# Kernel optimization log

Hardware: AMD Instinct MI355X
Metric: run time of the kernel (lower is better)

## Reference

```python
import jax, jax.numpy as jnp
import numpy as np

EPS = 1e-4  # ProtoPNet epsilon in distance-to-similarity transform


def setup_inputs() -> dict:
    key = jax.random.key(0)
    k1, k2, k3 = jax.random.split(key, 3)
    B, C, T = 128, 128, 777   # backbone feature map [B, C, T]
    P, NC = 500, 5            # prototypes, classes
    x = jax.random.normal(k1, (B, C, T), dtype=jnp.float32)
    prototypes = jax.random.uniform(k2, (P, C), dtype=jnp.float32)
    last_w = jax.random.normal(k3, (P, NC), dtype=jnp.float32)
    return {"x": x, "prototypes": prototypes, "last_w": last_w}


def reference(x, prototypes, last_w):
    # Prototype layer via the conv-trick L2 expansion:
    x2 = jnp.sum(x * x, axis=1)                      # [B, T]
    p2 = jnp.sum(prototypes * prototypes, axis=1)    # [P]
    xp = jnp.einsum('bct,pc->bpt', x, prototypes)    # [B, P, T]  (dominant GEMM)
    d = jnp.maximum(x2[:, None, :] - 2.0 * xp + p2[None, :, None], 0.0)  # [B, P, T]
    # Min-pool over all patches (global min over temporal axis)
    min_d = jnp.min(d, axis=2)                       # [B, P]
    # Distance -> similarity: log((d + 1) / (d + eps))
    sim = jnp.log((min_d + 1.0) / (min_d + EPS))     # [B, P]
    # Final evidence layer
    logits = sim @ last_w                            # [B, num_classes]
    return logits
```

## Files before the change

kernel.cpp:

```cpp
#include <hip/hip_runtime.h>
#include <hip/hip_bf16.h>

#define B_DIM 128
#define C_DIM 128
#define T_DIM 777
#define P_DIM 500
#define P_PAD 512
#define NCLS  5
#define EPSV  1e-4f
#define NT    25

typedef unsigned short u16;
typedef unsigned int   u32;
typedef __attribute__((ext_vector_type(8))) short short8;
typedef __attribute__((ext_vector_type(4))) float f32x4;
typedef float float4u __attribute__((ext_vector_type(4), aligned(4)));

__device__ __forceinline__ u32 cvt_pk_bf16(float a, float b) {
    u32 r;
    asm("v_cvt_pk_bf16_f32 %0, %1, %2" : "=v"(r) : "v"(a), "v"(b));
    return r;
}

__global__ __launch_bounds__(256, 3) void fused_gemm_min(
    const float* __restrict__ x,
    const float* __restrict__ proto,
    float* __restrict__ wsmin) {

    const int o   = blockIdx.x;
    const int xcd = o & 7, j = o >> 3;
    const int bl  = j / 6;
    const int r6  = j - bl * 6;
    const int b   = xcd * 16 + bl;
    const int pt  = r6 & 1;
    const int th  = r6 >> 1;
    const int it0 = (th == 0) ? 0 : (th == 1 ? 9 : 17);
    const int itN = (th == 0) ? 9 : (th == 1 ? 17 : NT);

    const int tid = threadIdx.x;
    const int w = tid >> 6, l = tid & 63;
    const int row16 = l & 15, kq = l >> 4;
    const int wp = pt * 256 + w * 64;

    const int c0  = (tid >> 3) << 2;
    const int tl0 = (tid & 7) << 2;

    __shared__ __align__(16) char  smem[2][32 * 256];
    __shared__ __align__(16) float x2p[2][4][32];

    const float* xb = x + (size_t)b * C_DIM * T_DIM;

    short8 afr[4][4];
#pragma unroll
    for (int ps = 0; ps < 4; ++ps) {
        const int r = wp + ps * 16 + row16;
#pragma unroll
        for (int kst = 0; kst < 4; ++kst) {
            const int k0 = kst * 32 + kq * 8;
            union { short8 s; u32 d[4]; } t;
            if (r < P_DIM) {
                float4 u0 = *(const float4*)(proto + r * C_DIM + k0);
                float4 u1 = *(const float4*)(proto + r * C_DIM + k0 + 4);
                t.d[0] = cvt_pk_bf16(u0.x, u0.y);
                t.d[1] = cvt_pk_bf16(u0.z, u0.w);
                t.d[2] = cvt_pk_bf16(u1.x, u1.y);
                t.d[3] = cvt_pk_bf16(u1.z, u1.w);
            } else {
                t.d[0] = t.d[1] = t.d[2] = t.d[3] = 0u;
            }
            afr[ps][kst] = t.s;
        }
    }

    float vb[4][4];
    auto loadv = [&](int it) {
        const int tb = it * 32 + tl0;
        if (tb + 3 < T_DIM) {
#pragma unroll
            for (int r = 0; r < 4; ++r) {
                float4u u = *(const float4u*)(xb + (c0 + r) * T_DIM + tb);
                vb[r][0]=u[0]; vb[r][1]=u[1]; vb[r][2]=u[2]; vb[r][3]=u[3];
            }
        } else {
#pragma unroll
            for (int r = 0; r < 4; ++r)
#pragma unroll
                for (int jj = 0; jj < 4; ++jj) {
                    const int t = tb + jj;
                    vb[r][jj] = (t < T_DIM) ? xb[(c0 + r) * T_DIM + t] : 0.f;
                }
        }
    };

    auto write_tile = [&](int it, int bsel) {
        const int t0 = it * 32;
        float s[4];
#pragma unroll
        for (int jj = 0; jj < 4; ++jj)
            s[jj] = vb[0][jj]*vb[0][jj] + vb[1][jj]*vb[1][jj]
                  + vb[2][jj]*vb[2][jj] + vb[3][jj]*vb[3][jj];
#pragma unroll
        for (int jj = 0; jj < 4; ++jj) {
            const u32 lo = cvt_pk_bf16(vb[0][jj], vb[1][jj]);
            const u32 hi = cvt_pk_bf16(vb[2][jj], vb[3][jj]);
            const int tl  = tl0 + jj;
            const int off = tl * 256 + (((c0 >> 3) ^ (tl & 7)) << 4) + ((c0 & 4) << 1);
            *(uint2*)(smem[bsel] + off) = make_uint2(lo, hi);
        }
#pragma unroll
        for (int m = 8; m <= 32; m <<= 1)
#pragma unroll
            for (int jj = 0; jj < 4; ++jj) s[jj] += __shfl_xor(s[jj], m);
        if ((l >> 3) == 0) {
            float4 o4;
            o4.x = (t0 + tl0 + 0 < T_DIM) ? s[0] : 1e30f;
            o4.y = (t0 + tl0 + 1 < T_DIM) ? s[1] : 1e30f;
            o4.z = (t0 + tl0 + 2 < T_DIM) ? s[2] : 1e30f;
            o4.w = (t0 + tl0 + 3 < T_DIM) ? s[3] : 1e30f;
            *(float4*)(&x2p[bsel][w][tl0]) = o4;
        }
    };

    f32x4 minv[4];
#pragma unroll
    for (int ps = 0; ps < 4; ++ps) minv[ps] = (f32x4){1e30f, 1e30f, 1e30f, 1e30f};

    loadv(it0);
    write_tile(it0, 0);
    __syncthreads();

    int cur = 0;
    for (int it = it0; it < itN; ++it) {
        const bool more = (it + 1 < itN);
        if (more) loadv(it + 1);

        f32x4 acc[4][2];
#pragma unroll
        for (int ps = 0; ps < 4; ++ps)
#pragma unroll
            for (int ts = 0; ts < 2; ++ts) acc[ps][ts] = (f32x4){0.f, 0.f, 0.f, 0.f};

        const char* sbase = smem[cur];
        __builtin_amdgcn_s_setprio(1);
#pragma unroll
        for (int kst = 0; kst < 4; ++kst) {
            short8 bfr[2];
#pragma unroll
            for (int ts = 0; ts < 2; ++ts) {
                const int tl = ts * 16 + row16;
                const int gr = (kst * 4 + kq) ^ (tl & 7);
                bfr[ts] = *(const short8*)(sbase + tl * 256 + (gr << 4));
            }
#pragma unroll
            for (int ps = 0; ps < 4; ++ps)
#pragma unroll
                for (int ts = 0; ts < 2; ++ts)
                    acc[ps][ts] = __builtin_amdgcn_mfma_f32_16x16x32_bf16(
                        afr[ps][kst], bfr[ts], acc[ps][ts], 0, 0, 0);
        }
        __builtin_amdgcn_s_setprio(0);

        const float x2v0 = x2p[cur][0][row16]      + x2p[cur][1][row16]
                         + x2p[cur][2][row16]      + x2p[cur][3][row16];
        const float x2v1 = x2p[cur][0][16 + row16] + x2p[cur][1][16 + row16]
                         + x2p[cur][2][16 + row16] + x2p[cur][3][16 + row16];
#pragma unroll
        for (int ps = 0; ps < 4; ++ps)
#pragma unroll
            for (int q = 0; q < 4; ++q) {
                minv[ps][q] = fminf(minv[ps][q], fmaf(-2.f, acc[ps][0][q], x2v0));
                minv[ps][q] = fminf(minv[ps][q], fmaf(-2.f, acc[ps][1][q], x2v1));
            }

        if (more) write_tile(it + 1, cur ^ 1);
        __syncthreads();
        cur ^= 1;
    }

#pragma unroll
    for (int m = 1; m <= 8; m <<= 1)
#pragma unroll
        for (int ps = 0; ps < 4; ++ps)
#pragma unroll
            for (int q = 0; q < 4; ++q)
                minv[ps][q] = fminf(minv[ps][q], __shfl_xor(minv[ps][q], m));

    if (row16 == 0) {
#pragma unroll
        for (int ps = 0; ps < 4; ++ps) {
            const int p = wp + ps * 16 + kq * 4;
            *(float4*)(&wsmin[((size_t)th * B_DIM + b) * P_PAD + p]) =
                make_float4(minv[ps][0], minv[ps][1], minv[ps][2], minv[ps][3]);
        }
    }
}

__global__ __launch_bounds__(256) void combine_logits(
    const float* __restrict__ proto, const float* __restrict__ lw,
    const float* __restrict__ wsmin, float* __restrict__ out) {
    const int b = blockIdx.x, tid = threadIdx.x;
    float a[NCLS] = {0.f, 0.f, 0.f, 0.f, 0.f};
    for (int p = tid; p < P_DIM; p += 256) {
        const float4* pr = (const float4*)(proto + p * C_DIM);
        float p2 = 0.f;
#pragma unroll
        for (int i = 0; i < 32; ++i) {
            float4 u = pr[i];
            p2 += u.x*u.x + u.y*u.y + u.z*u.z + u.w*u.w;
        }
        const float m0 = wsmin[(0 * B_DIM + b) * P_PAD + p];
        const float m1 = wsmin[(1 * B_DIM + b) * P_PAD + p];
        const float m2 = wsmin[(2 * B_DIM + b) * P_PAD + p];
        const float m  = fminf(fminf(m0, m1), m2);
        const float md = fmaxf(m + p2, 0.f);
        const float sim = logf((md + 1.f) / (md + EPSV));
#pragma unroll
        for (int n = 0; n < NCLS; ++n) a[n] = fmaf(sim, lw[p * NCLS + n], a[n]);
    }
#pragma unroll
    for (int m = 1; m <= 32; m <<= 1)
#pragma unroll
        for (int n = 0; n < NCLS; ++n) a[n] += __shfl_xor(a[n], m);
    __shared__ float red[4][NCLS];
    const int w = tid >> 6, l = tid & 63;
    if (l == 0) {
#pragma unroll
        for (int n = 0; n < NCLS; ++n) red[w][n] = a[n];
    }
    __syncthreads();
    if (tid < NCLS)
        out[b * NCLS + tid] = red[0][tid] + red[1][tid] + red[2][tid] + red[3][tid];
}

__global__ __launch_bounds__(256) void fallback_k(const float* __restrict__ x,
                                                  const float* __restrict__ proto,
                                                  const float* __restrict__ lw,
                                                  float* __restrict__ out) {
    __shared__ float x2s[T_DIM];
    __shared__ float sims[P_DIM];
    int b = blockIdx.x, tid = threadIdx.x;
    for (int t = tid; t < T_DIM; t += 256) {
        float a = 0.f;
        for (int c = 0; c < C_DIM; ++c) { float v = x[((size_t)b * C_DIM + c) * T_DIM + t]; a = fmaf(v, v, a); }
        x2s[t] = a;
    }
    __syncthreads();
    for (int p = tid; p < P_DIM; p += 256) {
        float p2 = 0.f;
        for (int c = 0; c < C_DIM; ++c) { float v = proto[p * C_DIM + c]; p2 = fmaf(v, v, p2); }
        float mind = 1e30f;
        for (int t = 0; t < T_DIM; ++t) {
            float xp = 0.f;
            for (int c = 0; c < C_DIM; ++c)
                xp = fmaf(x[((size_t)b * C_DIM + c) * T_DIM + t], proto[p * C_DIM + c], xp);
            float d = fmaxf(x2s[t] - 2.f * xp + p2, 0.f);
            mind = fminf(mind, d);
        }
        sims[p] = logf((mind + 1.f) / (mind + EPSV));
    }
    __syncthreads();
    if (tid < NCLS) {
        float a = 0.f;
        for (int p = 0; p < P_DIM; ++p) a = fmaf(sims[p], lw[p * NCLS + tid], a);
        out[b * NCLS + tid] = a;
    }
}

extern "C" void kernel_launch(void* const* d_in, const int* in_sizes, int n_in,
                              void* d_out, int out_size, void* d_ws, size_t ws_size,
                              hipStream_t stream) {
    const float* x     = (const float*)d_in[0];
    const float* proto = (const float*)d_in[1];
    const float* lw    = (const float*)d_in[2];
    float* out = (float*)d_out;

    const size_t need = (size_t)3 * B_DIM * P_PAD * sizeof(float);

    if (ws_size >= need) {
        float* wsmin = (float*)d_ws;
        fused_gemm_min<<<dim3(768), 256, 0, stream>>>(x, proto, wsmin);
        combine_logits<<<dim3(B_DIM), 256, 0, stream>>>(proto, lw, wsmin, out);
    } else {
        fallback_k<<<dim3(B_DIM), 256, 0, stream>>>(x, proto, lw, out);
    }
}
```

Baseline: 50.77 us.

## Split x preprocessing into separate bf16 transpose kernel feeding GEMM-min

Adds a prep kernel that converts x to bf16, transposes it to [B, T_pad, C] and computes per-position squared norms into workspace. The GEMM-min kernel then streams pre-swizzled int4 tiles straight into a single LDS buffer instead of converting fp32 strided data inline. This targets the per-block conversion and norm-reduction work and the uncoalesced fp32 loads inside the main loop. In exchange it adds a kernel launch and an extra round trip of about 27 MB through global memory, and drops the double-buffered LDS in favour of two barriers per iteration.

Measured after the change: 54.71 us. +7.7%, slower.

```diff
diff --git a/kernel.cpp b/kernel.cpp
--- a/kernel.cpp
+++ b/kernel.cpp
@@ -4,17 +4,23 @@
 #define B_DIM 128
 #define C_DIM 128
 #define T_DIM 777
+#define T_PAD 832
 #define P_DIM 500
 #define P_PAD 512
 #define NCLS  5
 #define EPSV  1e-4f
-#define NT    25
+#define NTILE 26
 
 typedef unsigned short u16;
 typedef unsigned int   u32;
 typedef __attribute__((ext_vector_type(8))) short short8;
 typedef __attribute__((ext_vector_type(4))) float f32x4;
-typedef float float4u __attribute__((ext_vector_type(4), aligned(4)));
+
+__device__ __forceinline__ u16 f2bf(float f) {
+    u32 u = __float_as_uint(f);
+    u += 0x7FFFu + ((u >> 16) & 1u);
+    return (u16)(u >> 16);
+}
 
 __device__ __forceinline__ u32 cvt_pk_bf16(float a, float b) {
     u32 r;
@@ -22,8 +28,41 @@
     return r;
 }
 
-__global__ __launch_bounds__(256, 3) void fused_gemm_min(
-    const float* __restrict__ x,
+__global__ __launch_bounds__(256) void prep_x(const float* __restrict__ x,
+                                              u16* __restrict__ xbf,
+                                              float* __restrict__ x2) {
+    const int tc = blockIdx.x;
+    const int b  = blockIdx.y;
+    const int tid = threadIdx.x, w = tid >> 6, l = tid & 63;
+    __shared__ __align__(16) u16 xt[64][136];
+    const int t_loc = w * 16 + (l & 15);
+    const int cg = l >> 4;
+    const int t = tc * 64 + t_loc;
+    const float* xb = x + (size_t)b * C_DIM * T_DIM;
+    float acc = 0.f;
+#pragma unroll 8
+    for (int c0 = 0; c0 < C_DIM; c0 += 4) {
+        int c = c0 + cg;
+        float v = (t < T_DIM) ? xb[c * T_DIM + t] : 0.f;
+        acc = fmaf(v, v, acc);
+        xt[t_loc][c] = f2bf(v);
+    }
+    acc += __shfl_xor(acc, 16);
+    acc += __shfl_xor(acc, 32);
+    if (cg == 0) x2[b * T_PAD + t] = (t < T_DIM) ? acc : 1e30f;
+    __syncthreads();
+    int4* dst = (int4*)(xbf + ((size_t)b * T_PAD + tc * 64) * C_DIM);
+#pragma unroll
+    for (int q = 0; q < 4; ++q) {
+        int f = q * 256 + tid;
+        int tr = f >> 4, g = f & 15;
+        dst[f] = *(const int4*)((const char*)xt + tr * 272 + g * 16);
+    }
+}
+
+__global__ __launch_bounds__(256, 3) void gemm_min(
+    const int4* __restrict__ xg,
+    const float* __restrict__ x2,
     const float* __restrict__ proto,
     float* __restrict__ wsmin) {
 
@@ -35,20 +74,14 @@
     const int pt  = r6 & 1;
     const int th  = r6 >> 1;
     const int it0 = (th == 0) ? 0 : (th == 1 ? 9 : 17);
-    const int itN = (th == 0) ? 9 : (th == 1 ? 17 : NT);
+    const int itN = (th == 0) ? 9 : (th == 1 ? 17 : NTILE);
 
     const int tid = threadIdx.x;
     const int w = tid >> 6, l = tid & 63;
     const int row16 = l & 15, kq = l >> 4;
     const int wp = pt * 256 + w * 64;
 
-    const int c0  = (tid >> 3) << 2;
-    const int tl0 = (tid & 7) << 2;
-
-    __shared__ __align__(16) char  smem[2][32 * 256];
-    __shared__ __align__(16) float x2p[2][4][32];
-
-    const float* xb = x + (size_t)b * C_DIM * T_DIM;
+    __shared__ __align__(16) char smem[32 * 256];
 
     short8 afr[4][4];
 #pragma unroll
@@ -72,67 +105,33 @@
         }
     }
 
-    float vb[4][4];
-    auto loadv = [&](int it) {
-        const int tb = it * 32 + tl0;
-        if (tb + 3 < T_DIM) {
-#pragma unroll
-            for (int r = 0; r < 4; ++r) {
-                float4u u = *(const float4u*)(xb + (c0 + r) * T_DIM + tb);
-                vb[r][0]=u[0]; vb[r][1]=u[1]; vb[r][2]=u[2]; vb[r][3]=u[3];
-            }
-        } else {
-#pragma unroll
-            for (int r = 0; r < 4; ++r)
-#pragma unroll
-                for (int jj = 0; jj < 4; ++jj) {
-                    const int t = tb + jj;
-                    vb[r][jj] = (t < T_DIM) ? xb[(c0 + r) * T_DIM + t] : 0.f;
-                }
-        }
-    };
-
-    auto write_tile = [&](int it, int bsel) {
-        const int t0 = it * 32;
-        float s[4];
-#pragma unroll
-        for (int jj = 0; jj < 4; ++jj)
-            s[jj] = vb[0][jj]*vb[0][jj] + vb[1][jj]*vb[1][jj]
-                  + vb[2][jj]*vb[2][jj] + vb[3][jj]*vb[3][jj];
-#pragma unroll
-        for (int jj = 0; jj < 4; ++jj) {
-            const u32 lo = cvt_pk_bf16(vb[0][jj], vb[1][jj]);
-            const u32 hi = cvt_pk_bf16(vb[2][jj], vb[3][jj]);
-            const int tl  = tl0 + jj;
-            const int off = tl * 256 + (((c0 >> 3) ^ (tl & 7)) << 4) + ((c0 & 4) << 1);
-            *(uint2*)(smem[bsel] + off) = make_uint2(lo, hi);
-        }
-#pragma unroll
-        for (int m = 8; m <= 32; m <<= 1)
-#pragma unroll
-            for (int jj = 0; jj < 4; ++jj) s[jj] += __shfl_xor(s[jj], m);
-        if ((l >> 3) == 0) {
-            float4 o4;
-            o4.x = (t0 + tl0 + 0 < T_DIM) ? s[0] : 1e30f;
-            o4.y = (t0 + tl0 + 1 < T_DIM) ? s[1] : 1e30f;
-            o4.z = (t0 + tl0 + 2 < T_DIM) ? s[2] : 1e30f;
-            o4.w = (t0 + tl0 + 3 < T_DIM) ? s[3] : 1e30f;
-            *(float4*)(&x2p[bsel][w][tl0]) = o4;
-        }
-    };
+    const int d0 = (tid >> 4) * 256 + ((((tid & 15) ^ ((tid >> 4) & 7))) << 4);
+    const int d1 = d0 + 4096;
+    const int4* gb = xg + (size_t)b * T_PAD * 16;
+    const float* x2b = x2 + b * T_PAD;
 
     f32x4 minv[4];
 #pragma unroll
     for (int ps = 0; ps < 4; ++ps) minv[ps] = (f32x4){1e30f, 1e30f, 1e30f, 1e30f};
 
-    loadv(it0);
-    write_tile(it0, 0);
-    __syncthreads();
-
-    int cur = 0;
+    int4 v0 = gb[it0 * 512 + tid];
+    int4 v1 = gb[it0 * 512 + 256 + tid];
+    float xa = x2b[it0 * 32 + row16];
+    float xc = x2b[it0 * 32 + 16 + row16];
+
     for (int it = it0; it < itN; ++it) {
-        const bool more = (it + 1 < itN);
-        if (more) loadv(it + 1);
+        __syncthreads();
+        *(int4*)(smem + d0) = v0;
+        *(int4*)(smem + d1) = v1;
+        __syncthreads();
+
+        const float cxa = xa, cxc = xc;
+        if (it + 1 < itN) {
+            v0 = gb[(it + 1) * 512 + tid];
+            v1 = gb[(it + 1) * 512 + 256 + tid];
+            xa = x2b[(it + 1) * 32 + row16];
+            xc = x2b[(it + 1) * 32 + 16 + row16];
+        }
 
         f32x4 acc[4][2];
 #pragma unroll
@@ -140,7 +139,6 @@
 #pragma unroll
             for (int ts = 0; ts < 2; ++ts) acc[ps][ts] = (f32x4){0.f, 0.f, 0.f, 0.f};
 
-        const char* sbase = smem[cur];
         __builtin_amdgcn_s_setprio(1);
 #pragma unroll
         for (int kst = 0; kst < 4; ++kst) {
@@ -149,7 +147,7 @@
             for (int ts = 0; ts < 2; ++ts) {
                 const int tl = ts * 16 + row16;
                 const int gr = (kst * 4 + kq) ^ (tl & 7);
-                bfr[ts] = *(const short8*)(sbase + tl * 256 + (gr << 4));
+                bfr[ts] = *(const short8*)(smem + tl * 256 + (gr << 4));
             }
 #pragma unroll
             for (int ps = 0; ps < 4; ++ps)
@@ -160,21 +158,13 @@
         }
         __builtin_amdgcn_s_setprio(0);
 
-        const float x2v0 = x2p[cur][0][row16]      + x2p[cur][1][row16]
-                         + x2p[cur][2][row16]      + x2p[cur][3][row16];
-        const float x2v1 = x2p[cur][0][16 + row16] + x2p[cur][1][16 + row16]
-                         + x2p[cur][2][16 + row16] + x2p[cur][3][16 + row16];
 #pragma unroll
         for (int ps = 0; ps < 4; ++ps)
 #pragma unroll
             for (int q = 0; q < 4; ++q) {
-                minv[ps][q] = fminf(minv[ps][q], fmaf(-2.f, acc[ps][0][q], x2v0));
-                minv[ps][q] = fminf(minv[ps][q], fmaf(-2.f, acc[ps][1][q], x2v1));
+                minv[ps][q] = fminf(minv[ps][q], fmaf(-2.f, acc[ps][0][q], cxa));
+                minv[ps][q] = fminf(minv[ps][q], fmaf(-2.f, acc[ps][1][q], cxc));
             }
-
-        if (more) write_tile(it + 1, cur ^ 1);
-        __syncthreads();
-        cur ^= 1;
     }
 
 #pragma unroll
@@ -274,12 +264,18 @@
     const float* lw    = (const float*)d_in[2];
     float* out = (float*)d_out;
 
-    const size_t need = (size_t)3 * B_DIM * P_PAD * sizeof(float);
+    const size_t xbf_bytes = (size_t)B_DIM * T_PAD * C_DIM * 2;
+    const size_t x2_off  = xbf_bytes;
+    const size_t min_off = x2_off + (size_t)B_DIM * T_PAD * 4;
+    const size_t need    = min_off + (size_t)3 * B_DIM * P_PAD * 4;
 
     if (ws_size >= need) {
-        float* wsmin = (float*)d_ws;
-        fused_gemm_min<<<dim3(768), 256, 0, stream>>>(x, proto, wsmin);
-        combine_logits<<<dim3(B_DIM), 256, 0, stream>>>(proto, lw, wsmin, out);
+        u16*   xbf   = (u16*)d_ws;
+        float* x2    = (float*)((char*)d_ws + x2_off);
+        float* wsmin = (float*)((char*)d_ws + min_off);
+        prep_x        <<<dim3(T_PAD / 64, B_DIM), 256, 0, stream>>>(x, xbf, x2);
+        gemm_min      <<<dim3(768),               256, 0, stream>>>((const int4*)xbf, x2, proto, wsmin);
+        combine_logits<<<dim3(B_DIM),             256, 0, stream>>>(proto, lw, wsmin, out);
     } else {
         fallback_k<<<dim3(B_DIM), 256, 0, stream>>>(x, proto, lw, out);
     }
```

## Use 64-wide T tiles, 2-way T split, and precompute x norms up front

Applied to the files above, without the earlier changes.

Widens each loop iteration's time tile from 32 to 64 columns, so each wave issues 16 MFMAs per k-step. It cuts the temporal split from three blocks to two, shrinking the grid from 768 to 512 blocks and the combine reads from three partial minima to two. Squared x norms are now computed in a prologue by a strided scalar loop over channels, not fused into the tile write. The double-buffered LDS is replaced with a single buffer guarded by two barriers per iteration. This lowers the per-tile overhead ratio but adds a serial, uncoalesced-ish prologue that rereads x, and it removes the overlap between the LDS write and compute.

Result: faster. 48.76 us (-4.0%).

```diff
diff --git a/kernel.cpp b/kernel.cpp
--- a/kernel.cpp
+++ b/kernel.cpp
@@ -8,7 +8,8 @@
 #define P_PAD 512
 #define NCLS  5
 #define EPSV  1e-4f
-#define NT    25
+#define NTILE 13
+#define SPLIT 7
 
 typedef unsigned short u16;
 typedef unsigned int   u32;
@@ -22,20 +23,19 @@
     return r;
 }
 
-__global__ __launch_bounds__(256, 3) void fused_gemm_min(
+__global__ __launch_bounds__(256, 2) void fused_gemm_min(
     const float* __restrict__ x,
     const float* __restrict__ proto,
     float* __restrict__ wsmin) {
 
     const int o   = blockIdx.x;
     const int xcd = o & 7, j = o >> 3;
-    const int bl  = j / 6;
-    const int r6  = j - bl * 6;
-    const int b   = xcd * 16 + bl;
-    const int pt  = r6 & 1;
-    const int th  = r6 >> 1;
-    const int it0 = (th == 0) ? 0 : (th == 1 ? 9 : 17);
-    const int itN = (th == 0) ? 9 : (th == 1 ? 17 : NT);
+    const int b   = xcd * 16 + (j >> 2);
+    const int pt  = (j >> 1) & 1, th = j & 1;
+    const int it0 = th ? SPLIT : 0;
+    const int itN = th ? NTILE : SPLIT;
+    const int tb0 = it0 * 64;
+    const int nT  = (itN - it0) * 64;
 
     const int tid = threadIdx.x;
     const int w = tid >> 6, l = tid & 63;
@@ -45,10 +45,25 @@
     const int c0  = (tid >> 3) << 2;
     const int tl0 = (tid & 7) << 2;
 
-    __shared__ __align__(16) char  smem[2][32 * 256];
-    __shared__ __align__(16) float x2p[2][4][32];
+    __shared__ __align__(16) char  smem[64 * 256];
+    __shared__ __align__(16) float x2s[448];
 
     const float* xb = x + (size_t)b * C_DIM * T_DIM;
+
+    for (int i = tid; i < nT; i += 256) {
+        const int t = tb0 + i;
+        float a = 0.f;
+        if (t < T_DIM) {
+#pragma unroll 8
+            for (int c = 0; c < C_DIM; ++c) {
+                const float v = xb[c * T_DIM + t];
+                a = fmaf(v, v, a);
+            }
+            x2s[i] = a;
+        } else {
+            x2s[i] = 1e30f;
+        }
+    }
 
     short8 afr[4][4];
 #pragma unroll
@@ -72,109 +87,90 @@
         }
     }
 
-    float vb[4][4];
+    float vb[2][4][4];
     auto loadv = [&](int it) {
-        const int tb = it * 32 + tl0;
-        if (tb + 3 < T_DIM) {
-#pragma unroll
-            for (int r = 0; r < 4; ++r) {
-                float4u u = *(const float4u*)(xb + (c0 + r) * T_DIM + tb);
-                vb[r][0]=u[0]; vb[r][1]=u[1]; vb[r][2]=u[2]; vb[r][3]=u[3];
-            }
-        } else {
-#pragma unroll
-            for (int r = 0; r < 4; ++r)
-#pragma unroll
-                for (int jj = 0; jj < 4; ++jj) {
-                    const int t = tb + jj;
-                    vb[r][jj] = (t < T_DIM) ? xb[(c0 + r) * T_DIM + t] : 0.f;
+#pragma unroll
+        for (int h = 0; h < 2; ++h) {
+            const int tb = it * 64 + h * 32 + tl0;
+            if (tb + 3 < T_DIM) {
+#pragma unroll
+                for (int r = 0; r < 4; ++r) {
+                    float4u u = *(const float4u*)(xb + (c0 + r) * T_DIM + tb);
+                    vb[h][r][0]=u[0]; vb[h][r][1]=u[1]; vb[h][r][2]=u[2]; vb[h][r][3]=u[3];
                 }
+            } else {
+#pragma unroll
+                for (int r = 0; r < 4; ++r)
+#pragma unroll
+                    for (int jj = 0; jj < 4; ++jj) {
+                        const int t = (tb + jj < T_DIM) ? (tb + jj) : (T_DIM - 1);
+                        vb[h][r][jj] = xb[(c0 + r) * T_DIM + t];
+                    }
+            }
         }
     };
 
-    auto write_tile = [&](int it, int bsel) {
-        const int t0 = it * 32;
-        float s[4];
-#pragma unroll
-        for (int jj = 0; jj < 4; ++jj)
-            s[jj] = vb[0][jj]*vb[0][jj] + vb[1][jj]*vb[1][jj]
-                  + vb[2][jj]*vb[2][jj] + vb[3][jj]*vb[3][jj];
-#pragma unroll
-        for (int jj = 0; jj < 4; ++jj) {
-            const u32 lo = cvt_pk_bf16(vb[0][jj], vb[1][jj]);
-            const u32 hi = cvt_pk_bf16(vb[2][jj], vb[3][jj]);
-            const int tl  = tl0 + jj;
-            const int off = tl * 256 + (((c0 >> 3) ^ (tl & 7)) << 4) + ((c0 & 4) << 1);
-            *(uint2*)(smem[bsel] + off) = make_uint2(lo, hi);
-        }
-#pragma unroll
-        for (int m = 8; m <= 32; m <<= 1)
-#pragma unroll
-            for (int jj = 0; jj < 4; ++jj) s[jj] += __shfl_xor(s[jj], m);
-        if ((l >> 3) == 0) {
-            float4 o4;
-            o4.x = (t0 + tl0 + 0 < T_DIM) ? s[0] : 1e30f;
-            o4.y = (t0 + tl0 + 1 < T_DIM) ? s[1] : 1e30f;
-            o4.z = (t0 + tl0 + 2 < T_DIM) ? s[2] : 1e30f;
-            o4.w = (t0 + tl0 + 3 < T_DIM) ? s[3] : 1e30f;
-            *(float4*)(&x2p[bsel][w][tl0]) = o4;
-        }
-    };
-
     f32x4 minv[4];
 #pragma unroll
     for (int ps = 0; ps < 4; ++ps) minv[ps] = (f32x4){1e30f, 1e30f, 1e30f, 1e30f};
 
+    __syncthreads();
     loadv(it0);
-    write_tile(it0, 0);
-    __syncthreads();
-
-    int cur = 0;
+
     for (int it = it0; it < itN; ++it) {
-        const bool more = (it + 1 < itN);
-        if (more) loadv(it + 1);
-
-        f32x4 acc[4][2];
+#pragma unroll
+        for (int h = 0; h < 2; ++h)
+#pragma unroll
+            for (int jj = 0; jj < 4; ++jj) {
+                const u32 lo = cvt_pk_bf16(vb[h][0][jj], vb[h][1][jj]);
+                const u32 hi = cvt_pk_bf16(vb[h][2][jj], vb[h][3][jj]);
+                const int tl  = h * 32 + tl0 + jj;
+                const int off = tl * 256 + (((c0 >> 3) ^ (tl & 7)) << 4) + ((c0 & 4) << 1);
+                *(uint2*)(smem + off) = make_uint2(lo, hi);
+            }
+        __syncthreads();
+
+        if (it + 1 < itN) loadv(it + 1);
+
+        float xv[4];
+#pragma unroll
+        for (int ts = 0; ts < 4; ++ts)
+            xv[ts] = x2s[(it - it0) * 64 + ts * 16 + row16];
+
+        f32x4 acc[4][4];
 #pragma unroll
         for (int ps = 0; ps < 4; ++ps)
 #pragma unroll
-            for (int ts = 0; ts < 2; ++ts) acc[ps][ts] = (f32x4){0.f, 0.f, 0.f, 0.f};
-
-        const char* sbase = smem[cur];
+            for (int ts = 0; ts < 4; ++ts) acc[ps][ts] = (f32x4){0.f, 0.f, 0.f, 0.f};
+
         __builtin_amdgcn_s_setprio(1);
 #pragma unroll
         for (int kst = 0; kst < 4; ++kst) {
-            short8 bfr[2];
-#pragma unroll
-            for (int ts = 0; ts < 2; ++ts) {
+            short8 bfr[4];
+#pragma unroll
+            for (int ts = 0; ts < 4; ++ts) {
                 const int tl = ts * 16 + row16;
                 const int gr = (kst * 4 + kq) ^ (tl & 7);
-                bfr[ts] = *(const short8*)(sbase + tl * 256 + (gr << 4));
+                bfr[ts] = *(const short8*)(smem + tl * 256 + (gr << 4));
             }
 #pragma unroll
             for (int ps = 0; ps < 4; ++ps)
 #pragma unroll
-                for (int ts = 0; ts < 2; ++ts)
+                for (int ts = 0; ts < 4; ++ts)
                     acc[ps][ts] = __builtin_amdgcn_mfma_f32_16x16x32_bf16(
                         afr[ps][kst], bfr[ts], acc[ps][ts], 0, 0, 0);
         }
         __builtin_amdgcn_s_setprio(0);
 
-        const float x2v0 = x2p[cur][0][row16]      + x2p[cur][1][row16]
-                         + x2p[cur][2][row16]      + x2p[cur][3][row16];
-        const float x2v1 = x2p[cur][0][16 + row16] + x2p[cur][1][16 + row16]
-                         + x2p[cur][2][16 + row16] + x2p[cur][3][16 + row16];
 #pragma unroll
         for (int ps = 0; ps < 4; ++ps)
 #pragma unroll
-            for (int q = 0; q < 4; ++q) {
-                minv[ps][q] = fminf(minv[ps][q], fmaf(-2.f, acc[ps][0][q], x2v0));
-                minv[ps][q] = fminf(minv[ps][q], fmaf(-2.f, acc[ps][1][q], x2v1));
-            }
-
-        if (more) write_tile(it + 1, cur ^ 1);
+            for (int ts = 0; ts < 4; ++ts)
+#pragma unroll
+                for (int q = 0; q < 4; ++q)
+                    minv[ps][q] = fminf(minv[ps][q], fmaf(-2.f, acc[ps][ts][q], xv[ts]));
+
         __syncthreads();
-        cur ^= 1;
     }
 
 #pragma unroll
@@ -210,8 +206,7 @@
         }
         const float m0 = wsmin[(0 * B_DIM + b) * P_PAD + p];
         const float m1 = wsmin[(1 * B_DIM + b) * P_PAD + p];
-        const float m2 = wsmin[(2 * B_DIM + b) * P_PAD + p];
-        const float m  = fminf(fminf(m0, m1), m2);
+        const float m  = fminf(m0, m1);
         const float md = fmaxf(m + p2, 0.f);
         const float sim = logf((md + 1.f) / (md + EPSV));
 #pragma unroll
@@ -274,11 +269,11 @@
     const float* lw    = (const float*)d_in[2];
     float* out = (float*)d_out;
 
-    const size_t need = (size_t)3 * B_DIM * P_PAD * sizeof(float);
+    const size_t need = (size_t)2 * B_DIM * P_PAD * sizeof(float);
 
     if (ws_size >= need) {
         float* wsmin = (float*)d_ws;
-        fused_gemm_min<<<dim3(768), 256, 0, stream>>>(x, proto, wsmin);
+        fused_gemm_min<<<dim3(512), 256, 0, stream>>>(x, proto, wsmin);
         combine_logits<<<dim3(B_DIM), 256, 0, stream>>>(proto, lw, wsmin, out);
     } else {
         fallback_k<<<dim3(B_DIM), 256, 0, stream>>>(x, proto, lw, out);
```

## Split time axis four ways and single-buffer LDS for higher occupancy

Applied to the files above, without the earlier changes.

The temporal axis is now split into four chunks instead of three, giving 1024 blocks, and launch bounds are raised to four blocks per SM. The LDS double buffer becomes a single buffer with an extra barrier per iteration. The combine kernel reduces four partial minima instead of three. The goal is more parallelism and occupancy, at the cost of losing load/compute overlap through the second buffer, an extra sync per tile, and more blocks that each redo the prototype fragment load.

After: 97.92 us. 92.9% more time.

```diff
diff --git a/kernel.cpp b/kernel.cpp
--- a/kernel.cpp
+++ b/kernel.cpp
@@ -22,20 +22,19 @@
     return r;
 }
 
-__global__ __launch_bounds__(256, 3) void fused_gemm_min(
+__global__ __launch_bounds__(256, 4) void fused_gemm_min(
     const float* __restrict__ x,
     const float* __restrict__ proto,
     float* __restrict__ wsmin) {
 
     const int o   = blockIdx.x;
     const int xcd = o & 7, j = o >> 3;
-    const int bl  = j / 6;
-    const int r6  = j - bl * 6;
-    const int b   = xcd * 16 + bl;
-    const int pt  = r6 & 1;
-    const int th  = r6 >> 1;
-    const int it0 = (th == 0) ? 0 : (th == 1 ? 9 : 17);
-    const int itN = (th == 0) ? 9 : (th == 1 ? 17 : NT);
+    const int b   = xcd * 16 + (j >> 3);
+    const int r   = j & 7;
+    const int pt  = r >> 2;
+    const int th  = r & 3;
+    const int it0 = (th == 0) ? 0 : (th == 1 ? 7 : (th == 2 ? 13 : 19));
+    const int itN = (th == 0) ? 7 : (th == 1 ? 13 : (th == 2 ? 19 : NT));
 
     const int tid = threadIdx.x;
     const int w = tid >> 6, l = tid & 63;
@@ -45,22 +44,22 @@
     const int c0  = (tid >> 3) << 2;
     const int tl0 = (tid & 7) << 2;
 
-    __shared__ __align__(16) char  smem[2][32 * 256];
-    __shared__ __align__(16) float x2p[2][4][32];
+    __shared__ __align__(16) char  smem[32 * 256];
+    __shared__ __align__(16) float x2p[4][32];
 
     const float* xb = x + (size_t)b * C_DIM * T_DIM;
 
     short8 afr[4][4];
 #pragma unroll
     for (int ps = 0; ps < 4; ++ps) {
-        const int r = wp + ps * 16 + row16;
+        const int rr = wp + ps * 16 + row16;
 #pragma unroll
         for (int kst = 0; kst < 4; ++kst) {
             const int k0 = kst * 32 + kq * 8;
             union { short8 s; u32 d[4]; } t;
-            if (r < P_DIM) {
-                float4 u0 = *(const float4*)(proto + r * C_DIM + k0);
-                float4 u1 = *(const float4*)(proto + r * C_DIM + k0 + 4);
+            if (rr < P_DIM) {
+                float4 u0 = *(const float4*)(proto + rr * C_DIM + k0);
+                float4 u1 = *(const float4*)(proto + rr * C_DIM + k0 + 4);
                 t.d[0] = cvt_pk_bf16(u0.x, u0.y);
                 t.d[1] = cvt_pk_bf16(u0.z, u0.w);
                 t.d[2] = cvt_pk_bf16(u1.x, u1.y);
@@ -77,22 +76,22 @@
         const int tb = it * 32 + tl0;
         if (tb + 3 < T_DIM) {
 #pragma unroll
-            for (int r = 0; r < 4; ++r) {
-                float4u u = *(const float4u*)(xb + (c0 + r) * T_DIM + tb);
-                vb[r][0]=u[0]; vb[r][1]=u[1]; vb[r][2]=u[2]; vb[r][3]=u[3];
+            for (int rr = 0; rr < 4; ++rr) {
+                float4u u = *(const float4u*)(xb + (c0 + rr) * T_DIM + tb);
+                vb[rr][0]=u[0]; vb[rr][1]=u[1]; vb[rr][2]=u[2]; vb[rr][3]=u[3];
             }
         } else {
 #pragma unroll
-            for (int r = 0; r < 4; ++r)
+            for (int rr = 0; rr < 4; ++rr)
 #pragma unroll
                 for (int jj = 0; jj < 4; ++jj) {
                     const int t = tb + jj;
-                    vb[r][jj] = (t < T_DIM) ? xb[(c0 + r) * T_DIM + t] : 0.f;
+                    vb[rr][jj] = (t < T_DIM) ? xb[(c0 + rr) * T_DIM + t] : 0.f;
                 }
         }
     };
 
-    auto write_tile = [&](int it, int bsel) {
+    auto write_tile = [&](int it) {
         const int t0 = it * 32;
         float s[4];
 #pragma unroll
@@ -105,7 +104,7 @@
             const u32 hi = cvt_pk_bf16(vb[2][jj], vb[3][jj]);
             const int tl  = tl0 + jj;
             const int off = tl * 256 + (((c0 >> 3) ^ (tl & 7)) << 4) + ((c0 & 4) << 1);
-            *(uint2*)(smem[bsel] + off) = make_uint2(lo, hi);
+            *(uint2*)(smem + off) = make_uint2(lo, hi);
         }
 #pragma unroll
         for (int m = 8; m <= 32; m <<= 1)
@@ -117,7 +116,7 @@
             o4.y = (t0 + tl0 + 1 < T_DIM) ? s[1] : 1e30f;
             o4.z = (t0 + tl0 + 2 < T_DIM) ? s[2] : 1e30f;
             o4.w = (t0 + tl0 + 3 < T_DIM) ? s[3] : 1e30f;
-            *(float4*)(&x2p[bsel][w][tl0]) = o4;
+            *(float4*)(&x2p[w][tl0]) = o4;
         }
     };
 
@@ -126,10 +125,9 @@
     for (int ps = 0; ps < 4; ++ps) minv[ps] = (f32x4){1e30f, 1e30f, 1e30f, 1e30f};
 
     loadv(it0);
-    write_tile(it0, 0);
-    __syncthreads();
-
-    int cur = 0;
+    write_tile(it0);
+    __syncthreads();
+
     for (int it = it0; it < itN; ++it) {
         const bool more = (it + 1 < itN);
         if (more) loadv(it + 1);
@@ -140,7 +138,6 @@
 #pragma unroll
             for (int ts = 0; ts < 2; ++ts) acc[ps][ts] = (f32x4){0.f, 0.f, 0.f, 0.f};
 
-        const char* sbase = smem[cur];
         __builtin_amdgcn_s_setprio(1);
 #pragma unroll
         for (int kst = 0; kst < 4; ++kst) {
@@ -149,7 +146,7 @@
             for (int ts = 0; ts < 2; ++ts) {
                 const int tl = ts * 16 + row16;
                 const int gr = (kst * 4 + kq) ^ (tl & 7);
-                bfr[ts] = *(const short8*)(sbase + tl * 256 + (gr << 4));
+                bfr[ts] = *(const short8*)(smem + tl * 256 + (gr << 4));
             }
 #pragma unroll
             for (int ps = 0; ps < 4; ++ps)
@@ -160,10 +157,10 @@
         }
         __builtin_amdgcn_s_setprio(0);
 
-        const float x2v0 = x2p[cur][0][row16]      + x2p[cur][1][row16]
-                         + x2p[cur][2][row16]      + x2p[cur][3][row16];
-        const float x2v1 = x2p[cur][0][16 + row16] + x2p[cur][1][16 + row16]
-                         + x2p[cur][2][16 + row16] + x2p[cur][3][16 + row16];
+        const float x2v0 = x2p[0][row16]      + x2p[1][row16]
+                         + x2p[2][row16]      + x2p[3][row16];
+        const float x2v1 = x2p[0][16 + row16] + x2p[1][16 + row16]
+                         + x2p[2][16 + row16] + x2p[3][16 + row16];
 #pragma unroll
         for (int ps = 0; ps < 4; ++ps)
 #pragma unroll
@@ -172,9 +169,11 @@
                 minv[ps][q] = fminf(minv[ps][q], fmaf(-2.f, acc[ps][1][q], x2v1));
             }
 
-        if (more) write_tile(it + 1, cur ^ 1);
         __syncthreads();
-        cur ^= 1;
+        if (more) {
+            write_tile(it + 1);
+            __syncthreads();
+        }
     }
 
 #pragma unroll
@@ -208,10 +207,11 @@
             float4 u = pr[i];
             p2 += u.x*u.x + u.y*u.y + u.z*u.z + u.w*u.w;
         }
-        const float m0 = wsmin[(0 * B_DIM + b) * P_PAD + p];
-        const float m1 = wsmin[(1 * B_DIM + b) * P_PAD + p];
-        const float m2 = wsmin[(2 * B_DIM + b) * P_PAD + p];
-        const float m  = fminf(fminf(m0, m1), m2);
+        const float m0 = wsmin[((size_t)0 * B_DIM + b) * P_PAD + p];
+        const float m1 = wsmin[((size_t)1 * B_DIM + b) * P_PAD + p];
+        const float m2 = wsmin[((size_t)2 * B_DIM + b) * P_PAD + p];
+        const float m3 = wsmin[((size_t)3 * B_DIM + b) * P_PAD + p];
+        const float m  = fminf(fminf(m0, m1), fminf(m2, m3));
         const float md = fmaxf(m + p2, 0.f);
         const float sim = logf((md + 1.f) / (md + EPSV));
 #pragma unroll
@@ -274,11 +274,11 @@
     const float* lw    = (const float*)d_in[2];
     float* out = (float*)d_out;
 
-    const size_t need = (size_t)3 * B_DIM * P_PAD * sizeof(float);
+    const size_t need = (size_t)4 * B_DIM * P_PAD * sizeof(float);
 
     if (ws_size >= need) {
         float* wsmin = (float*)d_ws;
-        fused_gemm_min<<<dim3(768), 256, 0, stream>>>(x, proto, wsmin);
+        fused_gemm_min<<<dim3(1024), 256, 0, stream>>>(x, proto, wsmin);
         combine_logits<<<dim3(B_DIM), 256, 0, stream>>>(proto, lw, wsmin, out);
     } else {
         fallback_k<<<dim3(B_DIM), 256, 0, stream>>>(x, proto, lw, out);
```
